# Performance work log

Measured on AMD Instinct MI355X. Metric: run time of the kernel, lower is better.

## Reference

```python
import jax, jax.numpy as jnp
import numpy as np

IN, H, T = 512, 1024, 1024


def _xavier(key, shape):
    a = (6.0 / (shape[0] + shape[1])) ** 0.5
    return jax.random.uniform(key, shape, minval=-a, maxval=a, dtype=jnp.float32)


def setup_inputs() -> dict:
    key = jax.random.key(0)
    ks = jax.random.split(key, 20)
    inp = {
        'x': jax.random.normal(ks[0], (1, T, IN), dtype=jnp.float32),
        'time': jax.random.uniform(ks[1], (T,), dtype=jnp.float32),
    }
    # initial states ~ N(0, 0.1) as in the source forward
    names = ['h0_1', 'c0_1', 'h0_2', 'c0_2', 'h0_3', 'c0_3']
    for i, n in enumerate(names):
        inp[n] = 0.1 * jax.random.normal(ks[2 + i], (1, H), dtype=jnp.float32)
    # LSTMCell params: weights xavier_uniform, biases uniform(0,1) (torch gate order i,f,g,o)
    inp['W_ih1'] = _xavier(ks[8], (4 * H, IN + 1))
    inp['W_hh1'] = _xavier(ks[9], (4 * H, H))
    inp['b_ih1'] = jax.random.uniform(ks[10], (4 * H,), dtype=jnp.float32)
    inp['b_hh1'] = jax.random.uniform(ks[11], (4 * H,), dtype=jnp.float32)
    inp['W_ih2'] = _xavier(ks[12], (4 * H, H))
    inp['W_hh2'] = _xavier(ks[13], (4 * H, H))
    inp['b_ih2'] = jax.random.uniform(ks[14], (4 * H,), dtype=jnp.float32)
    inp['b_hh2'] = jax.random.uniform(ks[15], (4 * H,), dtype=jnp.float32)
    return inp


def reference(x, time, h0_1, c0_1, h0_2, c0_2, h0_3, c0_3,
              W_ih1, W_hh1, b_ih1, b_hh1, W_ih2, W_hh2, b_ih2, b_hh2):
    def cell(xt, h, c, W_ih, W_hh, b_ih, b_hh):
        gates = xt @ W_ih.T + b_ih + h @ W_hh.T + b_hh  # (1, 4H)
        i, f, g, o = jnp.split(gates, 4, axis=-1)
        c_new = jax.nn.sigmoid(f) * c + jax.nn.sigmoid(i) * jnp.tanh(g)
        h_new = jax.nn.sigmoid(o) * jnp.tanh(c_new)
        return h_new, c_new

    xs = jnp.concatenate([x[0], time[:, None]], axis=1)  # (T, IN+1)

    def step(carry, xt):
        h1, c1, h2, c2, h3, c3 = carry
        h1, c1 = cell(xt[None, :], h1, c1, W_ih1, W_hh1, b_ih1, b_hh1)
        h2, c2 = cell(h1, h2, c2, W_ih2, W_hh2, b_ih2, b_hh2)
        # source calls self.lstm2 again for the third layer (lstm3 unused)
        h3, c3 = cell(h2, h3, c3, W_ih2, W_hh2, b_ih2, b_hh2)
        return (h1, c1, h2, c2, h3, c3), h3[0]

    carry, hs = jax.lax.scan(step, (h0_1, c0_1, h0_2, c0_2, h0_3, c0_3), xs)
    hs = hs[None]              # (1, T, H)
    h_final = carry[4]         # (1, H) -- last h3
    attn = jnp.einsum('bth,bh->bt', hs, h_final)
    w = jax.nn.softmax(attn, axis=1)
    context = jnp.einsum('bth,bt->bh', hs, w)  # (1, H)
    return context
```

## Files before the change

kernel.cpp:

```cpp
#include <hip/hip_runtime.h>
#include <hip/hip_fp16.h>

#define TSTEPS 1024
#define HDIM   1024
#define INDIM  512
#define NGATE  4096
#define NWG_L1  64
#define NWG_L23 128
#define NWG_TOT 192
#define POISON_U 0x7C7C7C7Cu
#define SPIN_MAX (1 << 20)


typedef _Float16 half2v __attribute__((ext_vector_type(2)));

#define PINU(v) asm volatile("" : "+v"(v))

__device__ __forceinline__ float dot2f(unsigned h, unsigned w, float c) {
    half2v a = __builtin_bit_cast(half2v, h);
    half2v b = __builtin_bit_cast(half2v, w);
    c = fmaf((float)a[0], (float)b[0], c);
    c = fmaf((float)a[1], (float)b[1], c);
    return c;
}

__device__ __forceinline__ float wave_sum64_dpp(float v) {
    int x;
    x = __builtin_amdgcn_update_dpp(0, __float_as_int(v), 0x111, 0xf, 0xf, false); v += __int_as_float(x);
    x = __builtin_amdgcn_update_dpp(0, __float_as_int(v), 0x112, 0xf, 0xf, false); v += __int_as_float(x);
    x = __builtin_amdgcn_update_dpp(0, __float_as_int(v), 0x114, 0xf, 0xf, false); v += __int_as_float(x);
    x = __builtin_amdgcn_update_dpp(0, __float_as_int(v), 0x118, 0xf, 0xf, false); v += __int_as_float(x);
    x = __builtin_amdgcn_update_dpp(0, __float_as_int(v), 0x142, 0xa, 0xf, false); v += __int_as_float(x);
    x = __builtin_amdgcn_update_dpp(0, __float_as_int(v), 0x143, 0xc, 0xf, false); v += __int_as_float(x);
    return v;
}

__device__ __forceinline__ float sigm(float x) { return 1.f / (1.f + __expf(-x)); }
__device__ __forceinline__ float fast_tanh(float x) {
    float t = __expf(-2.f * fabsf(x));
    float r = (1.f - t) / (1.f + t);
    return copysignf(r, x);
}

__device__ __forceinline__ unsigned pack_h(float a, float b) {
    auto p = __builtin_amdgcn_cvt_pkrtz(a, b);
    return __builtin_bit_cast(unsigned, p);
}

__device__ __forceinline__ unsigned agent_loadu(const unsigned* p) {
    return __hip_atomic_load(const_cast<unsigned*>(p), __ATOMIC_RELAXED,
                             __HIP_MEMORY_SCOPE_AGENT);
}
__device__ __forceinline__ void agent_storeu(unsigned* p, unsigned v) {
    __hip_atomic_store(p, v, __ATOMIC_RELAXED, __HIP_MEMORY_SCOPE_AGENT);
}

__global__ __launch_bounds__(256) void pack_f16(
    const float* __restrict__ src, unsigned* __restrict__ dst, int n)
{
    int i = blockIdx.x * 256 + threadIdx.x;
    if (i < n) {
        float2 v = *(const float2*)(src + 2 * (size_t)i);
        dst[i] = (unsigned)__half_as_ushort(__float2half(v.x)) |
                 ((unsigned)__half_as_ushort(__float2half(v.y)) << 16);
    }
}

#define BM 64
#define BN 64
#define BK 32

__global__ __launch_bounds__(256) void gemm_tn(
    const float* __restrict__ B,
    const float* __restrict__ bias1,
    const float* __restrict__ bias2,
    float* __restrict__ C,
    int M, int N, int K,
    const float* __restrict__ x,
    const float* __restrict__ timev)
{
    __shared__ float As[BK][BM + 4];
    __shared__ float Bs[BK][BN + 4];

    const int tid = threadIdx.x;
    const int mblocks = M / BM;
    const int bm = blockIdx.x % mblocks;
    const int bn = blockIdx.x / mblocks;
    const int t0 = bm * BM;
    const int n0 = bn * BN;

    const int tx = tid & 15;
    const int ty = tid >> 4;

    float acc[4][4] = {{0.f}};

    for (int kc = 0; kc < K; kc += BK) {
#pragma unroll
        for (int i = 0; i < 8; i++) {
            int idx = tid + i * 256;
            int r = idx >> 5;
            int c = idx & 31;
            int col = kc + c;
            int trow = t0 + r;
            float av = (col < INDIM) ? x[(size_t)trow * INDIM + col]
                                     : ((col == INDIM) ? timev[trow] : 0.f);
            As[c][r] = av;
            int nrow = n0 + r;
            Bs[c][r] = (col < K) ? B[(size_t)nrow * K + col] : 0.f;
        }
        __syncthreads();

#pragma unroll
        for (int kk = 0; kk < BK; kk++) {
            float a[4], b[4];
#pragma unroll
            for (int i = 0; i < 4; i++) a[i] = As[kk][ty * 4 + i];
#pragma unroll
            for (int j = 0; j < 4; j++) b[j] = Bs[kk][tx * 4 + j];
#pragma unroll
            for (int i = 0; i < 4; i++)
#pragma unroll
                for (int j = 0; j < 4; j++)
                    acc[i][j] = fmaf(a[i], b[j], acc[i][j]);
        }
        __syncthreads();
    }

#pragma unroll
    for (int i = 0; i < 4; i++) {
        int trow = t0 + ty * 4 + i;
#pragma unroll
        for (int j = 0; j < 4; j++) {
            int n = n0 + tx * 4 + j;
            C[(size_t)trow * N + n] = acc[i][j] + bias1[n] + bias2[n];
        }
    }
}

__global__ __launch_bounds__(1024, 4) void fused_scan(
    const unsigned* __restrict__ Wp1,
    const float* __restrict__ G1,
    const unsigned* __restrict__ Wpi2,
    const unsigned* __restrict__ Wph2,
    const float* bih2, const float* bhh2,
    const float* h0_1, const float* c0_1,
    const float* h0_2, const float* c0_2,
    const float* h0_3, const float* c0_3,
    unsigned* H1p, unsigned* H2p, unsigned* H3p,
    float* H3f)
{
    __shared__ unsigned shp1[512];
    __shared__ unsigned shp2[512];
    __shared__ unsigned shp3[512];
    __shared__ float gbuf[16][4];

    const int tid = threadIdx.x;
    const int wg  = blockIdx.x;
    const int q   = tid >> 6;
    const int s   = tid & 63;

    if (wg < NWG_L1) {
        const int u0 = wg << 4;
        const int u  = u0 + q;
        unsigned w[4][8];
#pragma unroll
        for (int g = 0; g < 4; ++g) {
            const unsigned* row = Wp1 + (size_t)((g << 10) + u) * 512 + s;
#pragma unroll
            for (int m = 0; m < 8; ++m)
                w[g][m] = row[64 * m];
        }
        float c1 = (tid < 16) ? c0_1[u0 + tid] : 0.f;
        unsigned pv = 0u;

        for (int t = 0; t < TSTEPS; ++t) {
#pragma unroll
            for (int g = 0; g < 4; ++g)
#pragma unroll
                for (int m = 0; m < 8; ++m) PINU(w[g][m]);

            float Gv0 = 0.f, Gv1 = 0.f, Gv2 = 0.f, Gv3 = 0.f;
            if (tid < 16) {
                const float* gptr = G1 + (size_t)t * NGATE + u0 + tid;
                Gv0 = gptr[0];
                Gv1 = gptr[1024];
                Gv2 = gptr[2048];
                Gv3 = gptr[3072];
            }
            if (tid < 512) {
                if (t == 0) {
                    shp1[tid] = pack_h(h0_1[2 * tid], h0_1[2 * tid + 1]);
                } else {
                    const unsigned* p = H1p + (size_t)(t - 1) * 512 + tid;
                    unsigned v = pv;
                    for (int it = 0; it < SPIN_MAX; ++it) {
                        if (__ballot(v == POISON_U) == 0ULL) break;
                        __builtin_amdgcn_s_sleep(1);
                        if (v == POISON_U) v = agent_loadu(p);
                    }
                    shp1[tid] = v;
                }
            }
            __syncthreads();

            float a0 = 0.f, a1 = 0.f, a2 = 0.f, a3 = 0.f;
#pragma unroll
            for (int m = 0; m < 8; ++m) {
                unsigned hu = shp1[s + 64 * m];
                a0 = dot2f(hu, w[0][m], a0);
                a1 = dot2f(hu, w[1][m], a1);
                a2 = dot2f(hu, w[2][m], a2);
                a3 = dot2f(hu, w[3][m], a3);
            }
            a0 = wave_sum64_dpp(a0);
            a1 = wave_sum64_dpp(a1);
            a2 = wave_sum64_dpp(a2);
            a3 = wave_sum64_dpp(a3);
            if (s == 63) {
                gbuf[q][0] = a0;
                gbuf[q][1] = a1;
                gbuf[q][2] = a2;
                gbuf[q][3] = a3;
            }
            __syncthreads();

            if (tid < 16) {
                float gi = gbuf[tid][0] + Gv0;
                float gf = gbuf[tid][1] + Gv1;
                float gg = gbuf[tid][2] + Gv2;
                float go = gbuf[tid][3] + Gv3;
                float i_ = sigm(gi), f_ = sigm(gf), g_ = fast_tanh(gg), o_ = sigm(go);
                c1 = f_ * c1 + i_ * g_;
                float hn = o_ * fast_tanh(c1);
                float hnn = __shfl_down(hn, 1, 64);
                if (!(tid & 1))
                    agent_storeu(H1p + (size_t)t * 512 + (u0 >> 1) + (tid >> 1),
                                 pack_h(hn, hnn));
            }
            if (tid < 512 && t < TSTEPS - 1) {
                pv = agent_loadu(H1p + (size_t)t * 512 + tid);
                PINU(pv);
            }
        }
    } else {
        const int ul = q >> 1;
        const int gp = q & 1;
        const int u0 = (wg - NWG_L1) << 3;
        const int u  = u0 + ul;
        unsigned wi[2][8], wh[2][8];
#pragma unroll
        for (int j = 0; j < 2; ++j) {
            const unsigned* ri = Wpi2 + (size_t)(((2 * gp + j) << 10) + u) * 512 + s;
            const unsigned* rh = Wph2 + (size_t)(((2 * gp + j) << 10) + u) * 512 + s;
#pragma unroll
            for (int m = 0; m < 8; ++m) {
                wi[j][m] = ri[64 * m];
                wh[j][m] = rh[64 * m];
            }
        }
        float bias0 = 0.f, bias1v = 0.f, bias2v = 0.f, bias3 = 0.f, cst = 0.f;
        if (tid < 16) {
            int uu = u0 + (tid & 7);
            bias0  = bih2[uu]        + bhh2[uu];
            bias1v = bih2[1024 + uu] + bhh2[1024 + uu];
            bias2v = bih2[2048 + uu] + bhh2[2048 + uu];
            bias3  = bih2[3072 + uu] + bhh2[3072 + uu];
            cst = (tid < 8) ? c0_2[u0 + tid] : c0_3[u0 + tid - 8];
        }
        unsigned pv1 = 0u;
        if (tid < 512) pv1 = agent_loadu(H1p + tid);

        for (int t = 0; t <= TSTEPS; ++t) {
#pragma unroll
            for (int j = 0; j < 2; ++j)
#pragma unroll
                for (int m = 0; m < 8; ++m) { PINU(wi[j][m]); PINU(wh[j][m]); }

            const bool do2 = (t < TSTEPS);
            const bool do3 = (t >= 1);

            if (tid < 512 && do2) {
                const unsigned* p = H1p + (size_t)t * 512 + tid;
                unsigned v = pv1;
                for (int it = 0; it < SPIN_MAX; ++it) {
                    if (__ballot(v == POISON_U) == 0ULL) break;
                    __builtin_amdgcn_s_sleep(1);
                    if (v == POISON_U) v = agent_loadu(p);
                }
                shp1[tid] = v;
            }
            __syncthreads();

            float p20 = 0.f, p21 = 0.f;
#pragma unroll
            for (int m = 0; m < 8; ++m) {
                unsigned h1u = shp1[s + 64 * m];
                p20 = dot2f(h1u, wi[0][m], p20);
                p21 = dot2f(h1u, wi[1][m], p21);
            }

            if (tid < 512) {
                if (t == 0) {
                    shp2[tid] = pack_h(h0_2[2 * tid], h0_2[2 * tid + 1]);
                } else {
                    const unsigned* p = H2p + (size_t)(t - 1) * 512 + tid;
                    unsigned v = agent_loadu(p);
                    for (int it = 0; it < SPIN_MAX; ++it) {
                        if (__ballot(v == POISON_U) == 0ULL) break;
                        __builtin_amdgcn_s_sleep(1);
                        if (v == POISON_U) v = agent_loadu(p);
                    }
                    shp2[tid] = v;
                }
            } else {
                const int sid = tid - 512;
                if (t == 1) {
                    shp3[sid] = pack_h(h0_3[2 * sid], h0_3[2 * sid + 1]);
                } else if (t > 1) {
                    const unsigned* p = H3p + (size_t)(t - 2) * 512 + sid;
                    unsigned v = agent_loadu(p);
                    for (int it = 0; it < SPIN_MAX; ++it) {
                        if (__ballot(v == POISON_U) == 0ULL) break;
                        __builtin_amdgcn_s_sleep(1);
                        if (v == POISON_U) v = agent_loadu(p);
                    }
                    shp3[sid] = v;
                }
            }
            __syncthreads();

            float p30 = 0.f, p31 = 0.f;
#pragma unroll
            for (int m = 0; m < 8; ++m) {
                unsigned h2u = shp2[s + 64 * m];
                unsigned h3u = shp3[s + 64 * m];
                p20 = dot2f(h2u, wh[0][m], p20);
                p21 = dot2f(h2u, wh[1][m], p21);
                p30 = dot2f(h2u, wi[0][m], p30);
                p31 = dot2f(h2u, wi[1][m], p31);
                p30 = dot2f(h3u, wh[0][m], p30);
                p31 = dot2f(h3u, wh[1][m], p31);
            }
            float s20 = wave_sum64_dpp(p20);
            float s21 = wave_sum64_dpp(p21);
            float s30 = wave_sum64_dpp(p30);
            float s31 = wave_sum64_dpp(p31);
            if (s == 63) {
                gbuf[ul][2 * gp]          = s20;
                gbuf[ul][2 * gp + 1]      = s21;
                gbuf[8 + ul][2 * gp]      = s30;
                gbuf[8 + ul][2 * gp + 1]  = s31;
            }
            __syncthreads();

            if (tid < 16) {
                const bool act = (tid < 8) ? do2 : do3;
                float hn = 0.f;
                if (act) {
                    float gi = gbuf[tid][0] + bias0;
                    float gf = gbuf[tid][1] + bias1v;
                    float gg = gbuf[tid][2] + bias2v;
                    float go = gbuf[tid][3] + bias3;
                    float i_ = sigm(gi), f_ = sigm(gf), g_ = fast_tanh(gg), o_ = sigm(go);
                    cst = f_ * cst + i_ * g_;
                    hn = o_ * fast_tanh(cst);
                }
                float hnn = __shfl_down(hn, 1, 64);
                if (act) {
                    if (tid < 8) {
                        if (!(tid & 1))
                            agent_storeu(H2p + (size_t)t * 512 + (u0 >> 1) + (tid >> 1),
                                         pack_h(hn, hnn));
                    } else {
                        if (!(tid & 1))
                            agent_storeu(H3p + (size_t)(t - 1) * 512 + (u0 >> 1) + ((tid - 8) >> 1),
                                         pack_h(hn, hnn));
                        H3f[(size_t)(t - 1) * HDIM + u0 + (tid - 8)] = hn;
                    }
                }
            }
            if (tid < 512 && t < TSTEPS - 1) {
                pv1 = agent_loadu(H1p + (size_t)(t + 1) * 512 + tid);
                PINU(pv1);
            }
        }
    }
}

__global__ __launch_bounds__(256) void attn_dot(
    const float* __restrict__ H3, float* __restrict__ attn)
{
    const int t = blockIdx.x * 4 + (threadIdx.x >> 6);
    const int lane = threadIdx.x & 63;
    const float* hrow = H3 + (size_t)t * HDIM;
    const float* hf = H3 + (size_t)(TSTEPS - 1) * HDIM;
    float p = 0.f;
    for (int j = lane; j < HDIM; j += 64) p = fmaf(hrow[j], hf[j], p);
#pragma unroll
    for (int d = 32; d; d >>= 1) p += __shfl_down(p, d, 64);
    if (lane == 0) attn[t] = p;
}

__global__ __launch_bounds__(64) void softmax_1024(float* attn)
{
    const int lane = threadIdx.x;
    float vals[16];
    float m = -1e30f;
#pragma unroll
    for (int i = 0; i < 16; i++) {
        vals[i] = attn[lane + i * 64];
        m = fmaxf(m, vals[i]);
    }
#pragma unroll
    for (int d = 32; d; d >>= 1) m = fmaxf(m, __shfl_xor(m, d, 64));
    float s = 0.f;
#pragma unroll
    for (int i = 0; i < 16; i++) {
        vals[i] = expf(vals[i] - m);
        s += vals[i];
    }
#pragma unroll
    for (int d = 32; d; d >>= 1) s += __shfl_xor(s, d, 64);
    float inv = 1.f / s;
#pragma unroll
    for (int i = 0; i < 16; i++) attn[lane + i * 64] = vals[i] * inv;
}

__global__ __launch_bounds__(256) void context_kernel(
    const float* __restrict__ H3, const float* __restrict__ w,
    float* __restrict__ out)
{
    const int u = blockIdx.x * 4 + (threadIdx.x >> 6);
    const int lane = threadIdx.x & 63;
    float p = 0.f;
    for (int t = lane; t < TSTEPS; t += 64)
        p = fmaf(H3[(size_t)t * HDIM + u], w[t], p);
#pragma unroll
    for (int d = 32; d; d >>= 1) p += __shfl_down(p, d, 64);
    if (lane == 0) out[u] = p;
}

extern "C" void kernel_launch(void* const* d_in, const int* in_sizes, int n_in,
                              void* d_out, int out_size, void* d_ws, size_t ws_size,
                              hipStream_t stream)
{
    const float* x     = (const float*)d_in[0];
    const float* timev = (const float*)d_in[1];
    const float* h0_1  = (const float*)d_in[2];
    const float* c0_1  = (const float*)d_in[3];
    const float* h0_2  = (const float*)d_in[4];
    const float* c0_2  = (const float*)d_in[5];
    const float* h0_3  = (const float*)d_in[6];
    const float* c0_3  = (const float*)d_in[7];
    const float* Wih1  = (const float*)d_in[8];
    const float* Whh1  = (const float*)d_in[9];
    const float* bih1  = (const float*)d_in[10];
    const float* bhh1  = (const float*)d_in[11];
    const float* Wih2  = (const float*)d_in[12];
    const float* Whh2  = (const float*)d_in[13];
    const float* bih2  = (const float*)d_in[14];
    const float* bhh2  = (const float*)d_in[15];

    float* G      = (float*)d_ws;
    unsigned* H1p = (unsigned*)(G + (size_t)TSTEPS * NGATE);
    unsigned* H2p = H1p + (size_t)TSTEPS * 512;
    unsigned* H3p = H2p + (size_t)TSTEPS * 512;
    float* H3f    = (float*)(H3p + (size_t)TSTEPS * 512);
    float* attn   = H3f + (size_t)TSTEPS * HDIM;
    unsigned* Wp1  = (unsigned*)(attn + 1024);
    unsigned* Wpi2 = Wp1 + (size_t)NGATE * 512;
    unsigned* Wph2 = Wpi2 + (size_t)NGATE * 512;
    float* out  = (float*)d_out;

    hipMemsetAsync(H1p, 0x7C, (size_t)3 * TSTEPS * 512 * sizeof(unsigned), stream);

    {
        const int n = NGATE * 512;
        pack_f16<<<dim3(n / 256), dim3(256), 0, stream>>>(Whh1, Wp1, n);
        pack_f16<<<dim3(n / 256), dim3(256), 0, stream>>>(Wih2, Wpi2, n);
        pack_f16<<<dim3(n / 256), dim3(256), 0, stream>>>(Whh2, Wph2, n);
    }

    gemm_tn<<<dim3(1024), dim3(256), 0, stream>>>(Wih1, bih1, bhh1, G,
                                                  TSTEPS, NGATE, INDIM + 1, x, timev);

    {
        const unsigned* a0 = Wp1;  const float* a1 = G;
        const unsigned* a2 = Wpi2; const unsigned* a3 = Wph2;
        const float* a4 = bih2;  const float* a5 = bhh2;
        const float* a6 = h0_1;  const float* a7 = c0_1;
        const float* a8 = h0_2;  const float* a9 = c0_2;
        const float* a10 = h0_3; const float* a11 = c0_3;
        unsigned* a12 = H1p; unsigned* a13 = H2p; unsigned* a14 = H3p;
        float* a15 = H3f;
        void* args[] = {&a0,&a1,&a2,&a3,&a4,&a5,&a6,&a7,&a8,&a9,&a10,&a11,
                        &a12,&a13,&a14,&a15};
        hipLaunchCooperativeKernel((void*)fused_scan, dim3(NWG_TOT), dim3(1024),
                                   args, 0, stream);
    }

    attn_dot<<<dim3(256), dim3(256), 0, stream>>>(H3f, attn);
    softmax_1024<<<dim3(1), dim3(64), 0, stream>>>(attn);
    context_kernel<<<dim3(256), dim3(256), 0, stream>>>(H3f, attn, out);
}
```

Before: 3.145 ms.

## Fuse input-projection GEMM into persistent scan kernel with poison-flag sync

Removes the separate gemm_tn launch. The 128 layer-2/3 workgroups of the cooperative scan kernel now compute the layer-1 input-projection tiles before they start their own recurrence. G is poisoned with memset, and layer-1 workgroups spin on each gate value until it becomes valid, so the GEMM overlaps with the start of the scan. It also swaps the scalar half-to-float FMA dot product for the fdot2 builtin when the compiler has it. This adds LDS use, extra spin-wait latency risk, and a large memset over G.

Result: faster. 2.784 ms (-11.5%).

```diff
diff --git a/kernel.cpp b/kernel.cpp
--- a/kernel.cpp
+++ b/kernel.cpp
@@ -13,9 +13,22 @@
 
 
 typedef _Float16 half2v __attribute__((ext_vector_type(2)));
+typedef decltype(__builtin_amdgcn_cvt_pkrtz(0.f, 0.f)) f16x2b;
 
 #define PINU(v) asm volatile("" : "+v"(v))
 
+#if defined(__has_builtin)
+#if __has_builtin(__builtin_amdgcn_fdot2)
+#define HAVE_FDOT2 1
+#endif
+#endif
+
+#ifdef HAVE_FDOT2
+__device__ __forceinline__ float dot2f(unsigned h, unsigned w, float c) {
+    return __builtin_amdgcn_fdot2(__builtin_bit_cast(f16x2b, h),
+                                  __builtin_bit_cast(f16x2b, w), c, false);
+}
+#else
 __device__ __forceinline__ float dot2f(unsigned h, unsigned w, float c) {
     half2v a = __builtin_bit_cast(half2v, h);
     half2v b = __builtin_bit_cast(half2v, w);
@@ -23,6 +36,7 @@
     c = fmaf((float)a[1], (float)b[1], c);
     return c;
 }
+#endif
 
 __device__ __forceinline__ float wave_sum64_dpp(float v) {
     int x;
@@ -54,6 +68,14 @@
 __device__ __forceinline__ void agent_storeu(unsigned* p, unsigned v) {
     __hip_atomic_store(p, v, __ATOMIC_RELAXED, __HIP_MEMORY_SCOPE_AGENT);
 }
+__device__ __forceinline__ float agent_loadf(const float* p) {
+    return __hip_atomic_load(const_cast<float*>(p), __ATOMIC_RELAXED,
+                             __HIP_MEMORY_SCOPE_AGENT);
+}
+__device__ __forceinline__ void agent_storef(float* p, float v) {
+    __hip_atomic_store(p, v, __ATOMIC_RELAXED, __HIP_MEMORY_SCOPE_AGENT);
+}
+__device__ __forceinline__ bool isp(float v) { return __float_as_uint(v) == POISON_U; }
 
 __global__ __launch_bounds__(256) void pack_f16(
     const float* __restrict__ src, unsigned* __restrict__ dst, int n)
@@ -69,35 +91,26 @@
 #define BM 64
 #define BN 64
 #define BK 32
-
-__global__ __launch_bounds__(256) void gemm_tn(
-    const float* __restrict__ B,
-    const float* __restrict__ bias1,
-    const float* __restrict__ bias2,
-    float* __restrict__ C,
-    int M, int N, int K,
-    const float* __restrict__ x,
-    const float* __restrict__ timev)
-{
-    __shared__ float As[BK][BM + 4];
-    __shared__ float Bs[BK][BN + 4];
-
-    const int tid = threadIdx.x;
-    const int mblocks = M / BM;
-    const int bm = blockIdx.x % mblocks;
-    const int bn = blockIdx.x / mblocks;
+#define GK (INDIM + 1)
+
+__device__ __forceinline__ void gemm_tile(
+    int bm, int bn, int ttid,
+    const float* __restrict__ B, const float* __restrict__ bias1,
+    const float* __restrict__ bias2, float* C,
+    const float* __restrict__ x, const float* __restrict__ timev,
+    float (*As)[BM + 4], float (*Bs)[BN + 4])
+{
     const int t0 = bm * BM;
     const int n0 = bn * BN;
-
-    const int tx = tid & 15;
-    const int ty = tid >> 4;
+    const int tx = ttid & 15;
+    const int ty = ttid >> 4;
 
     float acc[4][4] = {{0.f}};
 
-    for (int kc = 0; kc < K; kc += BK) {
+    for (int kc = 0; kc < GK; kc += BK) {
 #pragma unroll
         for (int i = 0; i < 8; i++) {
-            int idx = tid + i * 256;
+            int idx = ttid + i * 256;
             int r = idx >> 5;
             int c = idx & 31;
             int col = kc + c;
@@ -106,7 +119,7 @@
                                      : ((col == INDIM) ? timev[trow] : 0.f);
             As[c][r] = av;
             int nrow = n0 + r;
-            Bs[c][r] = (col < K) ? B[(size_t)nrow * K + col] : 0.f;
+            Bs[c][r] = (col < GK) ? B[(size_t)nrow * GK + col] : 0.f;
         }
         __syncthreads();
 
@@ -132,16 +145,20 @@
 #pragma unroll
         for (int j = 0; j < 4; j++) {
             int n = n0 + tx * 4 + j;
-            C[(size_t)trow * N + n] = acc[i][j] + bias1[n] + bias2[n];
+            agent_storef(C + (size_t)trow * NGATE + n,
+                         acc[i][j] + bias1[n] + bias2[n]);
         }
     }
 }
 
 __global__ __launch_bounds__(1024, 4) void fused_scan(
     const unsigned* __restrict__ Wp1,
-    const float* __restrict__ G1,
+    float* G1,
     const unsigned* __restrict__ Wpi2,
     const unsigned* __restrict__ Wph2,
+    const float* __restrict__ Wih1,
+    const float* __restrict__ bih1, const float* __restrict__ bhh1,
+    const float* __restrict__ xin, const float* __restrict__ timev,
     const float* bih2, const float* bhh2,
     const float* h0_1, const float* c0_1,
     const float* h0_2, const float* c0_2,
@@ -153,6 +170,8 @@
     __shared__ unsigned shp2[512];
     __shared__ unsigned shp3[512];
     __shared__ float gbuf[16][4];
+    __shared__ float AsT[4][BK][BM + 4];
+    __shared__ float BsT[4][BK][BN + 4];
 
     const int tid = threadIdx.x;
     const int wg  = blockIdx.x;
@@ -182,10 +201,10 @@
             float Gv0 = 0.f, Gv1 = 0.f, Gv2 = 0.f, Gv3 = 0.f;
             if (tid < 16) {
                 const float* gptr = G1 + (size_t)t * NGATE + u0 + tid;
-                Gv0 = gptr[0];
-                Gv1 = gptr[1024];
-                Gv2 = gptr[2048];
-                Gv3 = gptr[3072];
+                Gv0 = agent_loadf(gptr);
+                Gv1 = agent_loadf(gptr + 1024);
+                Gv2 = agent_loadf(gptr + 2048);
+                Gv3 = agent_loadf(gptr + 3072);
             }
             if (tid < 512) {
                 if (t == 0) {
@@ -225,6 +244,16 @@
             __syncthreads();
 
             if (tid < 16) {
+                const float* gptr = G1 + (size_t)t * NGATE + u0 + tid;
+                for (int it = 0; it < SPIN_MAX; ++it) {
+                    if (__ballot(isp(Gv0) | isp(Gv1) | isp(Gv2) | isp(Gv3)) == 0ULL)
+                        break;
+                    __builtin_amdgcn_s_sleep(1);
+                    if (isp(Gv0)) Gv0 = agent_loadf(gptr);
+                    if (isp(Gv1)) Gv1 = agent_loadf(gptr + 1024);
+                    if (isp(Gv2)) Gv2 = agent_loadf(gptr + 2048);
+                    if (isp(Gv3)) Gv3 = agent_loadf(gptr + 3072);
+                }
                 float gi = gbuf[tid][0] + Gv0;
                 float gf = gbuf[tid][1] + Gv1;
                 float gg = gbuf[tid][2] + Gv2;
@@ -243,6 +272,19 @@
             }
         }
     } else {
+        {
+            const int team = tid >> 8;
+            const int ttid = tid & 255;
+            const int tg   = (wg - NWG_L1) * 4 + team;
+#pragma unroll
+            for (int r = 0; r < 2; ++r) {
+                const int wk = tg + r * 512;
+                gemm_tile(wk >> 6, wk & 63, ttid, Wih1, bih1, bhh1, G1,
+                          xin, timev, AsT[team], BsT[team]);
+            }
+        }
+        __syncthreads();
+
         const int ul = q >> 1;
         const int gp = q & 1;
         const int u0 = (wg - NWG_L1) << 3;
@@ -472,7 +514,9 @@
     unsigned* Wph2 = Wpi2 + (size_t)NGATE * 512;
     float* out  = (float*)d_out;
 
-    hipMemsetAsync(H1p, 0x7C, (size_t)3 * TSTEPS * 512 * sizeof(unsigned), stream);
+    hipMemsetAsync(G, 0x7C,
+                   (size_t)TSTEPS * NGATE * sizeof(float) +
+                   (size_t)3 * TSTEPS * 512 * sizeof(unsigned), stream);
 
     {
         const int n = NGATE * 512;
@@ -481,20 +525,19 @@
         pack_f16<<<dim3(n / 256), dim3(256), 0, stream>>>(Whh2, Wph2, n);
     }
 
-    gemm_tn<<<dim3(1024), dim3(256), 0, stream>>>(Wih1, bih1, bhh1, G,
-                                                  TSTEPS, NGATE, INDIM + 1, x, timev);
-
     {
-        const unsigned* a0 = Wp1;  const float* a1 = G;
+        const unsigned* a0 = Wp1;  float* a1 = G;
         const unsigned* a2 = Wpi2; const unsigned* a3 = Wph2;
-        const float* a4 = bih2;  const float* a5 = bhh2;
-        const float* a6 = h0_1;  const float* a7 = c0_1;
-        const float* a8 = h0_2;  const float* a9 = c0_2;
-        const float* a10 = h0_3; const float* a11 = c0_3;
-        unsigned* a12 = H1p; unsigned* a13 = H2p; unsigned* a14 = H3p;
-        float* a15 = H3f;
+        const float* a4 = Wih1;  const float* a5 = bih1;  const float* a6 = bhh1;
+        const float* a7 = x;     const float* a8 = timev;
+        const float* a9 = bih2;  const float* a10 = bhh2;
+        const float* a11 = h0_1; const float* a12 = c0_1;
+        const float* a13 = h0_2; const float* a14 = c0_2;
+        const float* a15 = h0_3; const float* a16 = c0_3;
+        unsigned* a17 = H1p; unsigned* a18 = H2p; unsigned* a19 = H3p;
+        float* a20 = H3f;
         void* args[] = {&a0,&a1,&a2,&a3,&a4,&a5,&a6,&a7,&a8,&a9,&a10,&a11,
-                        &a12,&a13,&a14,&a15};
+                        &a12,&a13,&a14,&a15,&a16,&a17,&a18,&a19,&a20};
         hipLaunchCooperativeKernel((void*)fused_scan, dim3(NWG_TOT), dim3(1024),
                                    args, 0, stream);
     }
```
